# Optimization experiments

Hardware: AMD Instinct MI355X
Metric: run time of the kernel (lower is better)

The kernel has to match this reference:

```python
import jax, jax.numpy as jnp
import numpy as np

EMBED = 1024
HEADS = 16
HEAD_DIM = EMBED // HEADS

def setup_inputs() -> dict:
    key = jax.random.key(0)
    ks = jax.random.split(key, 5)
    B, S = 2, 2048
    scale = 1.0 / np.sqrt(EMBED)
    return {
        "query": jax.random.normal(ks[0], (B, S, EMBED), dtype=jnp.float32),
        "w_qkv": jax.random.normal(ks[1], (3 * EMBED, EMBED), dtype=jnp.float32) * scale,
        "b_qkv": jax.random.normal(ks[2], (3 * EMBED,), dtype=jnp.float32) * 0.01,
        "w_out": jax.random.normal(ks[3], (EMBED, EMBED), dtype=jnp.float32) * scale,
        "b_out": jax.random.normal(ks[4], (EMBED,), dtype=jnp.float32) * 0.01,
    }

def reference(query, w_qkv, b_qkv, w_out, b_out):
    B, S, E = query.shape
    H, D = HEADS, HEAD_DIM
    # fused qkv projection (torch Linear: x @ W.T + b)
    qkv = query @ w_qkv.T + b_qkv          # [B, S, 3E]
    q, k, v = jnp.split(qkv, 3, axis=-1)   # each [B, S, E]
    def heads(x):
        return x.reshape(B, S, H, D).transpose(0, 2, 1, 3)  # [B, H, S, D]
    q, k, v = heads(q), heads(k), heads(v)
    scale = D ** -0.5
    energy = jnp.einsum('bhqd,bhkd->bhqk', q, k) * scale    # [B, H, S, S]
    attn = jax.nn.softmax(energy, axis=-1)
    # dropout: inference mode (identity)
    out = jnp.einsum('bhqk,bhkd->bhqd', attn, v)            # [B, H, S, D]
    out = out.transpose(0, 2, 1, 3).reshape(B, S, E)
    return out @ w_out.T + b_out
```

## Files before the change

kernel.cpp:

```cpp
#include <hip/hip_runtime.h>
#include <hip/hip_bf16.h>
#include <cstdint>
#include <cstddef>


typedef float f32x4 __attribute__((ext_vector_type(4)));
typedef short s16x8 __attribute__((ext_vector_type(8)));

#define AS1C(p) ((const __attribute__((address_space(1))) void*)(p))
#define AS3(p)  ((__attribute__((address_space(3))) void*)(p))

__device__ __forceinline__ unsigned short f2bf(float f) {
    union { float f; unsigned u; } v; v.f = f;
    return (unsigned short)((v.u + 0x7FFFu + ((v.u >> 16) & 1u)) >> 16);
}

__device__ __forceinline__ float fast_exp2(float x) {
#if __has_builtin(__builtin_amdgcn_exp2f)
    return __builtin_amdgcn_exp2f(x);
#else
    return exp2f(x);
#endif
}

__global__ void cvt_bf16_3(const float* __restrict__ a, const float* __restrict__ b,
                           const float* __restrict__ c,
                           unsigned short* __restrict__ oa, unsigned short* __restrict__ ob,
                           unsigned short* __restrict__ oc,
                           int na4, int nb4, int nc4) {
    int j = blockIdx.x * blockDim.x + threadIdx.x;
    const float* s; unsigned short* d;
    if (j < na4) { s = a; d = oa; }
    else {
        j -= na4;
        if (j < nb4) { s = b; d = ob; }
        else { j -= nb4; if (j >= nc4) return; s = c; d = oc; }
    }
    float4 f = reinterpret_cast<const float4*>(s)[j];
    ushort4 o;
    o.x = f2bf(f.x); o.y = f2bf(f.y); o.z = f2bf(f.z); o.w = f2bf(f.w);
    reinterpret_cast<ushort4*>(d)[j] = o;
}

#define QSCALE_L2E (0.125f * 1.44269504088896f)

template <int MODE>
__global__ __launch_bounds__(256, 2)
void gemm_bt(const unsigned short* __restrict__ A,
             const unsigned short* __restrict__ B,
             const float* __restrict__ bias,
             float* __restrict__ Cf,
             unsigned short* __restrict__ Qw,
             unsigned short* __restrict__ Kw,
             unsigned short* __restrict__ Vtw,
             int M, int N, int K) {
    constexpr int BK = 32;
    __shared__ unsigned short As[128 * BK];
    __shared__ unsigned short Bs[128 * BK];

    const int tid = threadIdx.x;
    const int wid = tid >> 6, lane = tid & 63;
    const int brow = blockIdx.y * 128, bcol = blockIdx.x * 128;
    const int wr = wid >> 1, wc = wid & 1;

    f32x4 acc[4][4] = {};

    const int kIters = K / BK;
    for (int kt = 0; kt < kIters; ++kt) {
#pragma unroll
        for (int i = 0; i < 2; ++i) {
            const int lb = (wid * 2 + i) * 1024;
            const int row = (lb >> 6) + (lane >> 2);
            const int inrow = (lane & 3) * 16;
            const char* ga = (const char*)A + ((size_t)(brow + row) * K + kt * BK) * 2 + inrow;
            __builtin_amdgcn_global_load_lds(AS1C(ga), AS3((char*)As + lb), 16, 0, 0);
            const char* gb = (const char*)B + ((size_t)(bcol + row) * K + kt * BK) * 2 + inrow;
            __builtin_amdgcn_global_load_lds(AS1C(gb), AS3((char*)Bs + lb), 16, 0, 0);
        }
        __syncthreads();

        s16x8 af[4], bfr[4];
#pragma unroll
        for (int f = 0; f < 4; ++f) {
            af[f]  = *(const s16x8*)((const char*)As + (wr * 64 + f * 16 + (lane & 15)) * 64 + (lane >> 4) * 16);
            bfr[f] = *(const s16x8*)((const char*)Bs + (wc * 64 + f * 16 + (lane & 15)) * 64 + (lane >> 4) * 16);
        }
#pragma unroll
        for (int mf = 0; mf < 4; ++mf)
#pragma unroll
            for (int nf = 0; nf < 4; ++nf)
                acc[mf][nf] = __builtin_amdgcn_mfma_f32_16x16x32_bf16(af[mf], bfr[nf], acc[mf][nf], 0, 0, 0);
        __syncthreads();
    }

    float bv[4];
#pragma unroll
    for (int nf = 0; nf < 4; ++nf) bv[nf] = bias[bcol + wc * 64 + nf * 16 + (lane & 15)];

#pragma unroll
    for (int mf = 0; mf < 4; ++mf) {
#pragma unroll
        for (int r = 0; r < 4; ++r) {
            const int row = brow + wr * 64 + mf * 16 + (lane >> 4) * 4 + r;
#pragma unroll
            for (int nf = 0; nf < 4; ++nf) {
                const int col = bcol + wc * 64 + nf * 16 + (lane & 15);
                float v = acc[mf][nf][r] + bv[nf];
                if constexpr (MODE == 0) {
                    const int which = col >> 10, e = col & 1023;
                    const int h = e >> 6, d = e & 63;
                    const int b = row >> 11, s = row & 2047;
                    const size_t bh = (size_t)(b * 16 + h);
                    if (which == 0)      Qw[(bh * 2048 + s) * 64 + d] = f2bf(v * QSCALE_L2E);
                    else if (which == 1) Kw[(bh * 2048 + s) * 64 + d] = f2bf(v);
                    else                 Vtw[(bh * 64 + d) * 2048 + s] = f2bf(v);
                } else {
                    Cf[(size_t)row * N + col] = v;
                }
            }
        }
    }
}

__global__ __launch_bounds__(256, 4)
void attn_fwd(const unsigned short* __restrict__ Q,
              const unsigned short* __restrict__ Kk,
              const unsigned short* __restrict__ Vt,
              unsigned short* __restrict__ O) {
    __shared__ unsigned short Ks[2][64 * 64];
    __shared__ unsigned short Vs[2][64 * 64];
    __shared__ unsigned short Ps[4 * 16 * 64];

    const int tid = threadIdx.x;
    const int wid = tid >> 6, lane = tid & 63;

    const int bid = blockIdx.x;
    const int swzb = (bid & 7) * 128 + (bid >> 3);
    const int bh = swzb >> 5;
    const int qt = swzb & 31;
    const int b = bh >> 4, h = bh & 15;
    const int q0 = qt * 64 + wid * 16;

    const char* Qb  = (const char*)(Q  + (size_t)bh * 2048 * 64);
    const char* Kb  = (const char*)(Kk + (size_t)bh * 2048 * 64);
    const char* Vtb = (const char*)(Vt + (size_t)bh * 64 * 2048);
    char* PsW = (char*)Ps + wid * 2048;

    const int q = lane & 15, g = lane >> 4;
    const int qswz = (q & 7) << 4;

    s16x8 aq[2];
#pragma unroll
    for (int kf = 0; kf < 2; ++kf)
        aq[kf] = *(const s16x8*)(Qb + (size_t)(q0 + q) * 128 + (kf * 32 + g * 8) * 2);

    f32x4 o_acc[4] = {};
    f32x4 l_acc = {};
    s16x8 ones;
#pragma unroll
    for (int j = 0; j < 8; ++j) ones[j] = (short)0x3F80;

    auto stage = [&](int kc, int buf) {
#pragma unroll
        for (int i = 0; i < 2; ++i) {
            const int lb = (wid * 2 + i) * 1024;
            const int row = (lb >> 7) + (lane >> 3);
            const int inrow = (lane & 7) * 16;
            const int srcin = inrow ^ ((row & 7) << 4);
            const char* gk = Kb + (size_t)(kc * 64 + row) * 128 + srcin;
            __builtin_amdgcn_global_load_lds(AS1C(gk), AS3((char*)Ks[buf] + lb), 16, 0, 0);
            const char* gv = Vtb + (size_t)row * 4096 + kc * 128 + srcin;
            __builtin_amdgcn_global_load_lds(AS1C(gv), AS3((char*)Vs[buf] + lb), 16, 0, 0);
        }
    };

    stage(0, 0);
    __syncthreads();

    for (int kc = 0; kc < 32; ++kc) {
        const int cur = kc & 1;
        if (kc < 31) stage(kc + 1, cur ^ 1);

        f32x4 sacc[4];
#pragma unroll
        for (int nf = 0; nf < 4; ++nf) sacc[nf] = f32x4{-16.f, -16.f, -16.f, -16.f};
#pragma unroll
        for (int kf = 0; kf < 2; ++kf) {
            s16x8 bk[4];
#pragma unroll
            for (int nf = 0; nf < 4; ++nf) {
                const int key = nf * 16 + q;
                bk[nf] = *(const s16x8*)((const char*)Ks[cur] + key * 128 +
                                         (((kf * 32 + g * 8) * 2) ^ ((key & 7) << 4)));
            }
#pragma unroll
            for (int nf = 0; nf < 4; ++nf)
                sacc[nf] = __builtin_amdgcn_mfma_f32_16x16x32_bf16(bk[nf], aq[kf], sacc[nf], 0, 0, 0);
        }

        {
            char* pbase = PsW + q * 128;
#pragma unroll
            for (int nf = 0; nf < 4; ++nf) {
                float2 lo2 = make_float2(fast_exp2(sacc[nf][0]), fast_exp2(sacc[nf][1]));
                float2 hi2 = make_float2(fast_exp2(sacc[nf][2]), fast_exp2(sacc[nf][3]));
                __hip_bfloat162 plo = __float22bfloat162_rn(lo2);
                __hip_bfloat162 phi = __float22bfloat162_rn(hi2);
                uint2 w;
                w.x = *(unsigned*)&plo;
                w.y = *(unsigned*)&phi;
                const int cb = (nf * 16 + 4 * g) * 2;
                *(uint2*)(pbase + (cb ^ qswz)) = w;
            }
        }

        s16x8 pa[2];
#pragma unroll
        for (int kf = 0; kf < 2; ++kf)
            pa[kf] = *(const s16x8*)(PsW + q * 128 + (((kf * 32 + g * 8) * 2) ^ qswz));
#pragma unroll
        for (int kf = 0; kf < 2; ++kf) {
            l_acc = __builtin_amdgcn_mfma_f32_16x16x32_bf16(pa[kf], ones, l_acc, 0, 0, 0);
            s16x8 bv[4];
#pragma unroll
            for (int df = 0; df < 4; ++df) {
                const int drow = df * 16 + q;
                bv[df] = *(const s16x8*)((const char*)Vs[cur] + drow * 128 +
                                         (((kf * 32 + g * 8) * 2) ^ ((drow & 7) << 4)));
            }
#pragma unroll
            for (int df = 0; df < 4; ++df)
                o_acc[df] = __builtin_amdgcn_mfma_f32_16x16x32_bf16(pa[kf], bv[df], o_acc[df], 0, 0, 0);
        }
        __syncthreads();
    }

    float inv[4];
#pragma unroll
    for (int r = 0; r < 4; ++r) inv[r] = 1.f / l_acc[r];
#pragma unroll
    for (int df = 0; df < 4; ++df) {
#pragma unroll
        for (int r = 0; r < 4; ++r) {
            const int srow = q0 + g * 4 + r;
            const int dcol = df * 16 + q;
            O[(size_t)(b * 2048 + srow) * 1024 + h * 64 + dcol] = f2bf(o_acc[df][r] * inv[r]);
        }
    }
}

extern "C" void kernel_launch(void* const* d_in, const int* in_sizes, int n_in,
                              void* d_out, int out_size, void* d_ws, size_t ws_size,
                              hipStream_t stream) {
    const float* query = (const float*)d_in[0];
    const float* w_qkv = (const float*)d_in[1];
    const float* b_qkv = (const float*)d_in[2];
    const float* w_out = (const float*)d_in[3];
    const float* b_out = (const float*)d_in[4];
    float* out = (float*)d_out;

    unsigned short* ws = (unsigned short*)d_ws;
    unsigned short* Xbf    = ws;
    unsigned short* Wqkvbf = Xbf + 4096 * 1024;
    unsigned short* Woutbf = Wqkvbf + 3072 * 1024;
    unsigned short* Qw     = Woutbf + 1024 * 1024;
    unsigned short* Kw     = Qw + 32 * 2048 * 64;
    unsigned short* Vtw    = Kw + 32 * 2048 * 64;
    unsigned short* Obf    = Vtw + 32 * 2048 * 64;

    const int na4 = 4096 * 1024 / 4, nb4 = 3072 * 1024 / 4, nc4 = 1024 * 1024 / 4;
    cvt_bf16_3<<<(na4 + nb4 + nc4 + 255) / 256, 256, 0, stream>>>(
        query, w_qkv, w_out, Xbf, Wqkvbf, Woutbf, na4, nb4, nc4);

    gemm_bt<0><<<dim3(3072 / 128, 4096 / 128), 256, 0, stream>>>(
        Xbf, Wqkvbf, b_qkv, nullptr, Qw, Kw, Vtw, 4096, 3072, 1024);

    attn_fwd<<<dim3(1024), 256, 0, stream>>>(Qw, Kw, Vtw, Obf);

    gemm_bt<1><<<dim3(1024 / 128, 4096 / 128), 256, 0, stream>>>(
        Obf, Woutbf, b_out, out, nullptr, nullptr, nullptr, 4096, 1024, 1024);
}
```

Baseline: 132.5 us.

## Switch attention to 32x32x16 MFMA with register-level P transpose via permlane32_swap

The attention kernel moves from 16x16x32 to 32x32x16 bf16 MFMA tiles, with each wave handling 32 query rows and blocks shrunk to two waves. The softmax probabilities are rearranged into the MFMA A-operand layout in registers using v_permlane32_swap instead of a round trip through shared memory. The goal is to cut LDS traffic and instruction count per FLOP and to get more work per wave. The costs are fewer waves per block, higher register pressure from the 16-wide accumulators, and fewer threads sharing each K/V staging load.

```diff
diff --git a/kernel.cpp b/kernel.cpp
--- a/kernel.cpp
+++ b/kernel.cpp
@@ -4,8 +4,9 @@
 #include <cstddef>
 
 
-typedef float f32x4 __attribute__((ext_vector_type(4)));
-typedef short s16x8 __attribute__((ext_vector_type(8)));
+typedef float f32x4  __attribute__((ext_vector_type(4)));
+typedef float f32x16 __attribute__((ext_vector_type(16)));
+typedef short s16x8  __attribute__((ext_vector_type(8)));
 
 #define AS1C(p) ((const __attribute__((address_space(1))) void*)(p))
 #define AS3(p)  ((__attribute__((address_space(3))) void*)(p))
@@ -21,6 +22,19 @@
 #else
     return exp2f(x);
 #endif
+}
+
+__device__ __forceinline__ float fast_rcp(float x) {
+#if __has_builtin(__builtin_amdgcn_rcpf)
+    return __builtin_amdgcn_rcpf(x);
+#else
+    return 1.0f / x;
+#endif
+}
+
+__device__ __forceinline__ unsigned pk_bf2(float lo, float hi) {
+    __hip_bfloat162 p = __float22bfloat162_rn(make_float2(lo, hi));
+    return *(unsigned*)&p;
 }
 
 __global__ void cvt_bf16_3(const float* __restrict__ a, const float* __restrict__ b,
@@ -122,14 +136,13 @@
     }
 }
 
-__global__ __launch_bounds__(256, 4)
+__global__ __launch_bounds__(128, 2)
 void attn_fwd(const unsigned short* __restrict__ Q,
               const unsigned short* __restrict__ Kk,
               const unsigned short* __restrict__ Vt,
               unsigned short* __restrict__ O) {
     __shared__ unsigned short Ks[2][64 * 64];
     __shared__ unsigned short Vs[2][64 * 64];
-    __shared__ unsigned short Ps[4 * 16 * 64];
 
     const int tid = threadIdx.x;
     const int wid = tid >> 6, lane = tid & 63;
@@ -139,38 +152,35 @@
     const int bh = swzb >> 5;
     const int qt = swzb & 31;
     const int b = bh >> 4, h = bh & 15;
-    const int q0 = qt * 64 + wid * 16;
+    const int q0 = qt * 64 + wid * 32;
 
     const char* Qb  = (const char*)(Q  + (size_t)bh * 2048 * 64);
     const char* Kb  = (const char*)(Kk + (size_t)bh * 2048 * 64);
     const char* Vtb = (const char*)(Vt + (size_t)bh * 64 * 2048);
-    char* PsW = (char*)Ps + wid * 2048;
-
-    const int q = lane & 15, g = lane >> 4;
-    const int qswz = (q & 7) << 4;
-
-    s16x8 aq[2];
-#pragma unroll
-    for (int kf = 0; kf < 2; ++kf)
-        aq[kf] = *(const s16x8*)(Qb + (size_t)(q0 + q) * 128 + (kf * 32 + g * 8) * 2);
-
-    f32x4 o_acc[4] = {};
-    f32x4 l_acc = {};
+
+    const int x = lane & 31, hh = lane >> 5;
+
+    s16x8 aq[4];
+#pragma unroll
+    for (int kf = 0; kf < 4; ++kf)
+        aq[kf] = *(const s16x8*)(Qb + (size_t)(q0 + x) * 128 + (kf * 16 + hh * 8) * 2);
+
+    f32x16 o_acc[2] = {};
+    f32x16 l_acc = {};
     s16x8 ones;
 #pragma unroll
     for (int j = 0; j < 8; ++j) ones[j] = (short)0x3F80;
 
     auto stage = [&](int kc, int buf) {
 #pragma unroll
-        for (int i = 0; i < 2; ++i) {
-            const int lb = (wid * 2 + i) * 1024;
-            const int row = (lb >> 7) + (lane >> 3);
-            const int inrow = (lane & 7) * 16;
-            const int srcin = inrow ^ ((row & 7) << 4);
-            const char* gk = Kb + (size_t)(kc * 64 + row) * 128 + srcin;
-            __builtin_amdgcn_global_load_lds(AS1C(gk), AS3((char*)Ks[buf] + lb), 16, 0, 0);
-            const char* gv = Vtb + (size_t)row * 4096 + kc * 128 + srcin;
-            __builtin_amdgcn_global_load_lds(AS1C(gv), AS3((char*)Vs[buf] + lb), 16, 0, 0);
+        for (int i = 0; i < 4; ++i) {
+            const int s = wid * 4 + i;
+            const int row = s * 8 + (lane >> 3);
+            const int inrow = ((lane & 7) * 16) ^ ((row & 7) << 4);
+            const char* gk = Kb + (size_t)(kc * 64 + row) * 128 + inrow;
+            __builtin_amdgcn_global_load_lds(AS1C(gk), AS3((char*)Ks[buf] + s * 1024), 16, 0, 0);
+            const char* gv = Vtb + (size_t)row * 4096 + kc * 128 + inrow;
+            __builtin_amdgcn_global_load_lds(AS1C(gv), AS3((char*)Vs[buf] + s * 1024), 16, 0, 0);
         }
     };
 
@@ -181,70 +191,66 @@
         const int cur = kc & 1;
         if (kc < 31) stage(kc + 1, cur ^ 1);
 
-        f32x4 sacc[4];
-#pragma unroll
-        for (int nf = 0; nf < 4; ++nf) sacc[nf] = f32x4{-16.f, -16.f, -16.f, -16.f};
-#pragma unroll
-        for (int kf = 0; kf < 2; ++kf) {
-            s16x8 bk[4];
-#pragma unroll
-            for (int nf = 0; nf < 4; ++nf) {
-                const int key = nf * 16 + q;
-                bk[nf] = *(const s16x8*)((const char*)Ks[cur] + key * 128 +
-                                         (((kf * 32 + g * 8) * 2) ^ ((key & 7) << 4)));
-            }
-#pragma unroll
-            for (int nf = 0; nf < 4; ++nf)
-                sacc[nf] = __builtin_amdgcn_mfma_f32_16x16x32_bf16(bk[nf], aq[kf], sacc[nf], 0, 0, 0);
-        }
-
-        {
-            char* pbase = PsW + q * 128;
-#pragma unroll
-            for (int nf = 0; nf < 4; ++nf) {
-                float2 lo2 = make_float2(fast_exp2(sacc[nf][0]), fast_exp2(sacc[nf][1]));
-                float2 hi2 = make_float2(fast_exp2(sacc[nf][2]), fast_exp2(sacc[nf][3]));
-                __hip_bfloat162 plo = __float22bfloat162_rn(lo2);
-                __hip_bfloat162 phi = __float22bfloat162_rn(hi2);
-                uint2 w;
-                w.x = *(unsigned*)&plo;
-                w.y = *(unsigned*)&phi;
-                const int cb = (nf * 16 + 4 * g) * 2;
-                *(uint2*)(pbase + (cb ^ qswz)) = w;
-            }
-        }
-
-        s16x8 pa[2];
-#pragma unroll
-        for (int kf = 0; kf < 2; ++kf)
-            pa[kf] = *(const s16x8*)(PsW + q * 128 + (((kf * 32 + g * 8) * 2) ^ qswz));
-#pragma unroll
-        for (int kf = 0; kf < 2; ++kf) {
-            l_acc = __builtin_amdgcn_mfma_f32_16x16x32_bf16(pa[kf], ones, l_acc, 0, 0, 0);
-            s16x8 bv[4];
-#pragma unroll
-            for (int df = 0; df < 4; ++df) {
-                const int drow = df * 16 + q;
-                bv[df] = *(const s16x8*)((const char*)Vs[cur] + drow * 128 +
-                                         (((kf * 32 + g * 8) * 2) ^ ((drow & 7) << 4)));
-            }
-#pragma unroll
-            for (int df = 0; df < 4; ++df)
-                o_acc[df] = __builtin_amdgcn_mfma_f32_16x16x32_bf16(pa[kf], bv[df], o_acc[df], 0, 0, 0);
-        }
+        f32x16 sacc[2] = {};
+#pragma unroll
+        for (int kt2 = 0; kt2 < 2; ++kt2) {
+#pragma unroll
+            for (int kf = 0; kf < 4; ++kf) {
+                const s16x8 bk = *(const s16x8*)((const char*)Ks[cur] + (kt2 * 32 + x) * 128 +
+                                                 ((kf * 32 + hh * 16) ^ ((x & 7) << 4)));
+                sacc[kt2] = __builtin_amdgcn_mfma_f32_32x32x16_bf16(bk, aq[kf], sacc[kt2], 0, 0, 0);
+            }
+        }
+
+        unsigned p2x[8], p2y[8];
+#pragma unroll
+        for (int kt2 = 0; kt2 < 2; ++kt2)
+#pragma unroll
+            for (int c = 0; c < 4; ++c) {
+                p2x[kt2 * 4 + c] = pk_bf2(fast_exp2(sacc[kt2][4 * c + 0]), fast_exp2(sacc[kt2][4 * c + 1]));
+                p2y[kt2 * 4 + c] = pk_bf2(fast_exp2(sacc[kt2][4 * c + 2]), fast_exp2(sacc[kt2][4 * c + 3]));
+            }
+
+        s16x8 pa[2][2];
+#pragma unroll
+        for (int kt2 = 0; kt2 < 2; ++kt2)
+#pragma unroll
+            for (int cp = 0; cp < 2; ++cp) {
+                unsigned ax = p2x[kt2 * 4 + 2 * cp], bx = p2x[kt2 * 4 + 2 * cp + 1];
+                unsigned ay = p2y[kt2 * 4 + 2 * cp], by = p2y[kt2 * 4 + 2 * cp + 1];
+                asm("v_permlane32_swap_b32 %0, %1" : "+v"(ax), "+v"(bx));
+                asm("v_permlane32_swap_b32 %0, %1" : "+v"(ay), "+v"(by));
+                union { s16x8 v; unsigned u[4]; } u;
+                u.u[0] = ax; u.u[1] = ay; u.u[2] = bx; u.u[3] = by;
+                pa[kt2][cp] = u.v;
+            }
+
+#pragma unroll
+        for (int kt2 = 0; kt2 < 2; ++kt2)
+#pragma unroll
+            for (int cp = 0; cp < 2; ++cp) {
+                l_acc = __builtin_amdgcn_mfma_f32_32x32x16_bf16(pa[kt2][cp], ones, l_acc, 0, 0, 0);
+#pragma unroll
+                for (int dt = 0; dt < 2; ++dt) {
+                    const int row = dt * 32 + x;
+                    const s16x8 bv = *(const s16x8*)((const char*)Vs[cur] + row * 128 +
+                                                     ((kt2 * 64 + cp * 32 + hh * 16) ^ ((x & 7) << 4)));
+                    o_acc[dt] = __builtin_amdgcn_mfma_f32_32x32x16_bf16(pa[kt2][cp], bv, o_acc[dt], 0, 0, 0);
+                }
+            }
         __syncthreads();
     }
 
-    float inv[4];
-#pragma unroll
-    for (int r = 0; r < 4; ++r) inv[r] = 1.f / l_acc[r];
-#pragma unroll
-    for (int df = 0; df < 4; ++df) {
-#pragma unroll
-        for (int r = 0; r < 4; ++r) {
-            const int srow = q0 + g * 4 + r;
-            const int dcol = df * 16 + q;
-            O[(size_t)(b * 2048 + srow) * 1024 + h * 64 + dcol] = f2bf(o_acc[df][r] * inv[r]);
+    float inv[16];
+#pragma unroll
+    for (int r = 0; r < 16; ++r) inv[r] = fast_rcp(l_acc[r]);
+#pragma unroll
+    for (int dt = 0; dt < 2; ++dt) {
+#pragma unroll
+        for (int r = 0; r < 16; ++r) {
+            const int qrow = q0 + (r & 3) + 8 * (r >> 2) + 4 * hh;
+            const int d = dt * 32 + x;
+            O[(size_t)(b * 2048 + qrow) * 1024 + h * 64 + d] = f2bf(o_acc[dt][r] * inv[r]);
         }
     }
 }
@@ -275,7 +281,7 @@
     gemm_bt<0><<<dim3(3072 / 128, 4096 / 128), 256, 0, stream>>>(
         Xbf, Wqkvbf, b_qkv, nullptr, Qw, Kw, Vtw, 4096, 3072, 1024);
 
-    attn_fwd<<<dim3(1024), 256, 0, stream>>>(Qw, Kw, Vtw, Obf);
+    attn_fwd<<<dim3(1024), 128, 0, stream>>>(Qw, Kw, Vtw, Obf);
 
     gemm_bt<1><<<dim3(1024 / 128, 4096 / 128), 256, 0, stream>>>(
         Obf, Woutbf, b_out, out, nullptr, nullptr, nullptr, 4096, 1024, 1024);
```

Measured after the change: 135.0 us. No clear change (+1.9%).
